# Performance work log

Hardware: AMD Instinct MI355X
Metric: run time of the kernel (lower is better)

## Reference

```python
import jax, jax.numpy as jnp
import numpy as np

EPS = 1e-5          # InstanceNorm2d default eps
SLOPE = 0.01        # LeakyReLU default negative_slope
C = 256


def setup_inputs() -> dict:
    key = jax.random.key(0)
    k = jax.random.split(key, 5)
    B, H, W = 8, 128, 128
    x = jax.random.normal(k[0], (B, C, H, W), dtype=jnp.float32)
    # attn: Conv2d(C, C//4, 1, bias=False) then Conv2d(C//4, C, 1, bias=False)
    attn_w1 = jax.random.normal(k[1], (C // 4, C), dtype=jnp.float32) * (1.0 / np.sqrt(C))
    attn_w2 = jax.random.normal(k[2], (C, C // 4), dtype=jnp.float32) * (1.0 / np.sqrt(C // 4))
    # refine: depthwise Conv2d(C, C, 3, padding=1, groups=C) with bias
    refine_w = jax.random.normal(k[3], (C, 1, 3, 3), dtype=jnp.float32) * (1.0 / 3.0)
    refine_b = jax.random.normal(k[4], (C,), dtype=jnp.float32) * 0.01
    return {"x": x, "attn_w1": attn_w1, "attn_w2": attn_w2,
            "refine_w": refine_w, "refine_b": refine_b}


def reference(x, attn_w1, attn_w2, refine_w, refine_b):
    # The torch module runs pywt wavedec2 -> waverec2 on x[b,c].detach().
    # With db2 (symmetric mode) and H,W divisible by 2^level, waverec2 is a
    # perfect-reconstruction identity and interpolate to (H,W) is a no-op,
    # so x_wave == stop_gradient(x) exactly.
    xw = jax.lax.stop_gradient(x)

    # --- channel attention (squeeze-excite with 1x1 convs == GEMMs) ---
    p = jnp.mean(xw, axis=(2, 3))                      # [B, C] global avg pool
    h = jax.nn.leaky_relu(p @ attn_w1.T, SLOPE)        # [B, C//4]
    a = jax.nn.sigmoid(h @ attn_w2.T)                  # [B, C]
    y = xw * a[:, :, None, None]

    # --- depthwise 3x3 refine conv ---
    y = jax.lax.conv_general_dilated(
        y, refine_w, window_strides=(1, 1), padding='SAME',
        feature_group_count=C,
        dimension_numbers=('NCHW', 'OIHW', 'NCHW'))
    y = y + refine_b[None, :, None, None]

    # --- InstanceNorm2d (affine=False, biased variance) ---
    mu = jnp.mean(y, axis=(2, 3), keepdims=True)
    var = jnp.mean(jnp.square(y - mu), axis=(2, 3), keepdims=True)
    y = (y - mu) * jax.lax.rsqrt(var + EPS)

    return jax.nn.leaky_relu(y, SLOPE)
```

## Files before the change

kernel.cpp:

```cpp
#include <hip/hip_runtime.h>
#include <hip/hip_bf16.h>
#include <math.h>

#define NPLANE 2048
#define HW     16384
#define WW     128
#define SLOPE  0.01f
#define EPS    1e-5f

typedef float v4f __attribute__((ext_vector_type(4)));

__device__ __forceinline__ void load_row(const float* __restrict__ xp, int r,
                                         int c4, int lane32,
                                         float4& m, float& L, float& R) {
    int rc = r;
    if (rc < 0) rc = 0;
    if (rc > 127) rc = 127;
    const float va = (r == rc) ? 1.f : 0.f;
    float4 v = *(const float4*)(xp + rc * WW + c4);
    m.x = v.x * va; m.y = v.y * va; m.z = v.z * va; m.w = v.w * va;
    L = __shfl_up(m.w, 1, 64);
    if (lane32 == 0) L = 0.f;
    R = __shfl_down(m.x, 1, 64);
    if (lane32 == 31) R = 0.f;
}

#define CONV4(o0, o1, o2, o3)                                                \
    float o0 = w_0*L0   + w_1*m0.x + w_2*m0.y                                \
             + w_3*L1   + w_4*m1.x + w_5*m1.y                                \
             + w_6*L2   + w_7*m2.x + w_8*m2.y;                               \
    float o1 = w_0*m0.x + w_1*m0.y + w_2*m0.z                                \
             + w_3*m1.x + w_4*m1.y + w_5*m1.z                                \
             + w_6*m2.x + w_7*m2.y + w_8*m2.z;                               \
    float o2 = w_0*m0.y + w_1*m0.z + w_2*m0.w                                \
             + w_3*m1.y + w_4*m1.z + w_5*m1.w                                \
             + w_6*m2.y + w_7*m2.z + w_8*m2.w;                               \
    float o3 = w_0*m0.z + w_1*m0.w + w_2*R0                                  \
             + w_3*m1.z + w_4*m1.w + w_5*R1                                  \
             + w_6*m2.z + w_7*m2.w + w_8*R2

#define SLIDE() do { m0 = m1; L0 = L1; R0 = R1; m1 = m2; L1 = L2; R1 = R2; } while (0)

__global__ __launch_bounds__(256, 8) void k_stats(const float* __restrict__ x,
                                                  const float* __restrict__ rw,
                                                  float* __restrict__ p,
                                                  float* __restrict__ cstats) {
    const int plane = blockIdx.x;
    const int ch = plane & 255;
    const float* xp = x + (size_t)plane * HW;
    const int lane32 = threadIdx.x & 31;
    const int c4 = lane32 * 4;
    const int r0 = (threadIdx.x >> 5) * 16;

    const float w_0 = rw[ch*9+0], w_1 = rw[ch*9+1], w_2 = rw[ch*9+2];
    const float w_3 = rw[ch*9+3], w_4 = rw[ch*9+4], w_5 = rw[ch*9+5];
    const float w_6 = rw[ch*9+6], w_7 = rw[ch*9+7], w_8 = rw[ch*9+8];

    float4 m0, m1, m2;
    float L0, R0, L1, R1, L2, R2;
    load_row(xp, r0 - 1, c4, lane32, m0, L0, R0);
    load_row(xp, r0,     c4, lane32, m1, L1, R1);

    float xs = 0.f, s = 0.f, sq = 0.f;
#pragma unroll 4
    for (int j = 0; j < 16; ++j) {
        load_row(xp, r0 + j + 1, c4, lane32, m2, L2, R2);
        CONV4(o0, o1, o2, o3);
        s  += (o0 + o1) + (o2 + o3);
        sq += o0*o0 + o1*o1 + o2*o2 + o3*o3;
        xs += (m1.x + m1.y) + (m1.z + m1.w);
        SLIDE();
    }

#pragma unroll
    for (int off = 32; off; off >>= 1) {
        xs += __shfl_down(xs, off, 64);
        s  += __shfl_down(s,  off, 64);
        sq += __shfl_down(sq, off, 64);
    }
    __shared__ float red[12];
    const int wave = threadIdx.x >> 6, lane = threadIdx.x & 63;
    if (lane == 0) { red[wave] = xs; red[4+wave] = s; red[8+wave] = sq; }
    __syncthreads();
    if (threadIdx.x == 0) {
        p[plane]            = ((red[0]+red[1]) + (red[2]+red[3])) * (1.f/(float)HW);
        cstats[plane*2]     = (red[4]+red[5]) + (red[6]+red[7]);
        cstats[plane*2 + 1] = (red[8]+red[9]) + (red[10]+red[11]);
    }
}

__global__ __launch_bounds__(256, 8) void k_out(const float* __restrict__ x,
                                                const float* __restrict__ w1,
                                                const float* __restrict__ w2,
                                                const float* __restrict__ rw,
                                                const float* __restrict__ p,
                                                const float* __restrict__ cstats,
                                                float* __restrict__ out) {
    __shared__ float hs[64];
    __shared__ float sh_mean, sh_scale;
    const int plane = blockIdx.x;
    const int b = plane >> 8, ch = plane & 255;

    {
        const int j = threadIdx.x >> 2, part = threadIdx.x & 3;
        const float4* pr = (const float4*)(p  + b * 256 + part * 64);
        const float4* wr = (const float4*)(w1 + j * 256 + part * 64);
        float acc = 0.f;
#pragma unroll
        for (int k = 0; k < 16; ++k) {
            float4 pv = pr[k], wv = wr[k];
            acc += pv.x*wv.x + pv.y*wv.y + pv.z*wv.z + pv.w*wv.w;
        }
        acc += __shfl_xor(acc, 1, 64);
        acc += __shfl_xor(acc, 2, 64);
        if (part == 0) hs[j] = acc > 0.f ? acc : SLOPE * acc;
    }
    __syncthreads();
    if (threadIdx.x < 64) {
        float v = w2[ch * 64 + threadIdx.x] * hs[threadIdx.x];
#pragma unroll
        for (int off = 32; off; off >>= 1) v += __shfl_down(v, off, 64);
        if (threadIdx.x == 0) {
            const float a  = 1.f / (1.f + expf(-v));
            const float mc = cstats[plane*2] * (1.f/(float)HW);
            const float vc = cstats[plane*2 + 1] * (1.f/(float)HW) - mc * mc;
            sh_mean  = mc;
            sh_scale = a * rsqrtf(a * a * vc + EPS);
        }
    }

    const float w_0 = rw[ch*9+0], w_1 = rw[ch*9+1], w_2 = rw[ch*9+2];
    const float w_3 = rw[ch*9+3], w_4 = rw[ch*9+4], w_5 = rw[ch*9+5];
    const float w_6 = rw[ch*9+6], w_7 = rw[ch*9+7], w_8 = rw[ch*9+8];

    __syncthreads();
    const float mean_c = sh_mean, scale = sh_scale;

    const float* xp = x + (size_t)plane * HW;
    float* op = out + (size_t)plane * HW;
    const int lane32 = threadIdx.x & 31;
    const int c4 = lane32 * 4;
    const int r0 = (threadIdx.x >> 5) * 16;

    float4 m0, m1, m2;
    float L0, R0, L1, R1, L2, R2;
    load_row(xp, r0 - 1, c4, lane32, m0, L0, R0);
    load_row(xp, r0,     c4, lane32, m1, L1, R1);

#pragma unroll 4
    for (int j = 0; j < 16; ++j) {
        load_row(xp, r0 + j + 1, c4, lane32, m2, L2, R2);
        CONV4(o0, o1, o2, o3);
        v4f res;
        float t0 = scale * (o0 - mean_c); res.x = t0 > 0.f ? t0 : SLOPE * t0;
        float t1 = scale * (o1 - mean_c); res.y = t1 > 0.f ? t1 : SLOPE * t1;
        float t2 = scale * (o2 - mean_c); res.z = t2 > 0.f ? t2 : SLOPE * t2;
        float t3 = scale * (o3 - mean_c); res.w = t3 > 0.f ? t3 : SLOPE * t3;
        __builtin_nontemporal_store(res, (v4f*)(op + (r0 + j) * WW + c4));
        SLIDE();
    }
}

extern "C" void kernel_launch(void* const* d_in, const int* in_sizes, int n_in,
                              void* d_out, int out_size, void* d_ws, size_t ws_size,
                              hipStream_t stream) {
    const float* x  = (const float*)d_in[0];
    const float* w1 = (const float*)d_in[1];
    const float* w2 = (const float*)d_in[2];
    const float* rw = (const float*)d_in[3];
    float* out = (float*)d_out;

    float* p      = (float*)d_ws;
    float* cstats = p + NPLANE;

    k_stats<<<NPLANE, 256, 0, stream>>>(x, rw, p, cstats);
    k_out  <<<NPLANE, 256, 0, stream>>>(x, w1, w2, rw, p, cstats, out);
}
```

Before: 276.0 us.

## Fuse stats and output kernels into one cooperative launch with grid sync

The two kernels become one cooperative kernel. It computes the conv statistics per plane, waits at a grid-wide barrier, then runs the squeeze-excite and the normalized conv output in the same launch. This removes the second launch and may let the second pass over x hit in cache because the same blocks reread their planes. It relies on all 2048 blocks being co-resident (8 per CU on 256 CUs); if the cooperative launch fails, it falls back to the original two launches.

```diff
diff --git a/kernel.cpp b/kernel.cpp
--- a/kernel.cpp
+++ b/kernel.cpp
@@ -1,6 +1,8 @@
 #include <hip/hip_runtime.h>
-#include <hip/hip_bf16.h>
+#include <hip/hip_cooperative_groups.h>
 #include <math.h>
+
+namespace cg = cooperative_groups;
 
 #define NPLANE 2048
 #define HW     16384
@@ -41,6 +43,115 @@
 
 #define SLIDE() do { m0 = m1; L0 = L1; R0 = R1; m1 = m2; L1 = L2; R1 = R2; } while (0)
 
+__global__ __launch_bounds__(256, 8) void k_fused(const float* __restrict__ x,
+                                                  const float* __restrict__ w1,
+                                                  const float* __restrict__ w2,
+                                                  const float* __restrict__ rw,
+                                                  float* __restrict__ p,
+                                                  float* __restrict__ cstats,
+                                                  float* __restrict__ out) {
+    __shared__ float red[12];
+    __shared__ float hs[64];
+    __shared__ float sh_mean, sh_scale;
+
+    const int plane = blockIdx.x;
+    const int b = plane >> 8, ch = plane & 255;
+    const float* xp = x + (size_t)plane * HW;
+    const int lane32 = threadIdx.x & 31;
+    const int c4 = lane32 * 4;
+    const int r0 = (threadIdx.x >> 5) * 16;
+
+    const float w_0 = rw[ch*9+0], w_1 = rw[ch*9+1], w_2 = rw[ch*9+2];
+    const float w_3 = rw[ch*9+3], w_4 = rw[ch*9+4], w_5 = rw[ch*9+5];
+    const float w_6 = rw[ch*9+6], w_7 = rw[ch*9+7], w_8 = rw[ch*9+8];
+
+    {
+        float4 m0, m1, m2;
+        float L0, R0, L1, R1, L2, R2;
+        load_row(xp, r0 - 1, c4, lane32, m0, L0, R0);
+        load_row(xp, r0,     c4, lane32, m1, L1, R1);
+
+        float xs = 0.f, s = 0.f, sq = 0.f;
+#pragma unroll 4
+        for (int j = 0; j < 16; ++j) {
+            load_row(xp, r0 + j + 1, c4, lane32, m2, L2, R2);
+            CONV4(o0, o1, o2, o3);
+            s  += (o0 + o1) + (o2 + o3);
+            sq += o0*o0 + o1*o1 + o2*o2 + o3*o3;
+            xs += (m1.x + m1.y) + (m1.z + m1.w);
+            SLIDE();
+        }
+
+#pragma unroll
+        for (int off = 32; off; off >>= 1) {
+            xs += __shfl_down(xs, off, 64);
+            s  += __shfl_down(s,  off, 64);
+            sq += __shfl_down(sq, off, 64);
+        }
+        const int wave = threadIdx.x >> 6, lane = threadIdx.x & 63;
+        if (lane == 0) { red[wave] = xs; red[4+wave] = s; red[8+wave] = sq; }
+        __syncthreads();
+        if (threadIdx.x == 0) {
+            p[plane]            = ((red[0]+red[1]) + (red[2]+red[3])) * (1.f/(float)HW);
+            cstats[plane*2]     = (red[4]+red[5]) + (red[6]+red[7]);
+            cstats[plane*2 + 1] = (red[8]+red[9]) + (red[10]+red[11]);
+        }
+    }
+
+    cg::this_grid().sync();
+
+    {
+        const int j = threadIdx.x >> 2, part = threadIdx.x & 3;
+        const float4* pr = (const float4*)(p  + b * 256 + part * 64);
+        const float4* wr = (const float4*)(w1 + j * 256 + part * 64);
+        float acc = 0.f;
+#pragma unroll
+        for (int k = 0; k < 16; ++k) {
+            float4 pv = pr[k], wv = wr[k];
+            acc += pv.x*wv.x + pv.y*wv.y + pv.z*wv.z + pv.w*wv.w;
+        }
+        acc += __shfl_xor(acc, 1, 64);
+        acc += __shfl_xor(acc, 2, 64);
+        if (part == 0) hs[j] = acc > 0.f ? acc : SLOPE * acc;
+    }
+    __syncthreads();
+    if (threadIdx.x < 64) {
+        float v = w2[ch * 64 + threadIdx.x] * hs[threadIdx.x];
+#pragma unroll
+        for (int off = 32; off; off >>= 1) v += __shfl_down(v, off, 64);
+        if (threadIdx.x == 0) {
+            const float a  = 1.f / (1.f + expf(-v));
+            const float mc = cstats[plane*2] * (1.f/(float)HW);
+            const float vc = cstats[plane*2 + 1] * (1.f/(float)HW) - mc * mc;
+            sh_mean  = mc;
+            sh_scale = a * rsqrtf(a * a * vc + EPS);
+        }
+    }
+    __syncthreads();
+    const float mean_c = sh_mean, scale = sh_scale;
+
+    float* op = out + (size_t)plane * HW;
+    {
+        float4 m0, m1, m2;
+        float L0, R0, L1, R1, L2, R2;
+        load_row(xp, r0 - 1, c4, lane32, m0, L0, R0);
+        load_row(xp, r0,     c4, lane32, m1, L1, R1);
+
+#pragma unroll 4
+        for (int j = 0; j < 16; ++j) {
+            load_row(xp, r0 + j + 1, c4, lane32, m2, L2, R2);
+            CONV4(o0, o1, o2, o3);
+            v4f res;
+            float t0 = scale * (o0 - mean_c); res.x = t0 > 0.f ? t0 : SLOPE * t0;
+            float t1 = scale * (o1 - mean_c); res.y = t1 > 0.f ? t1 : SLOPE * t1;
+            float t2 = scale * (o2 - mean_c); res.z = t2 > 0.f ? t2 : SLOPE * t2;
+            float t3 = scale * (o3 - mean_c); res.w = t3 > 0.f ? t3 : SLOPE * t3;
+            __builtin_nontemporal_store(res, (v4f*)(op + (r0 + j) * WW + c4));
+            SLIDE();
+        }
+    }
+}
+
 __global__ __launch_bounds__(256, 8) void k_stats(const float* __restrict__ x,
                                                   const float* __restrict__ rw,
                                                   float* __restrict__ p,
@@ -173,6 +284,13 @@
     float* p      = (float*)d_ws;
     float* cstats = p + NPLANE;
 
-    k_stats<<<NPLANE, 256, 0, stream>>>(x, rw, p, cstats);
-    k_out  <<<NPLANE, 256, 0, stream>>>(x, w1, w2, rw, p, cstats, out);
-}
+    void* args[] = {(void*)&x, (void*)&w1, (void*)&w2, (void*)&rw,
+                    (void*)&p, (void*)&cstats, (void*)&out};
+    hipError_t e = hipLaunchCooperativeKernel((const void*)k_fused,
+                                              dim3(NPLANE), dim3(256),
+                                              args, 0, stream);
+    if (e != hipSuccess) {
+        k_stats<<<NPLANE, 256, 0, stream>>>(x, rw, p, cstats);
+        k_out  <<<NPLANE, 256, 0, stream>>>(x, w1, w2, rw, p, cstats, out);
+    }
+}
```

Measured after the change: 448.6 us. 1.63x slower.

## Move conv statistics into output kernel, keeping conv results in registers

Applied to the files above, without the earlier changes.

The first kernel now only computes the per-plane mean of x with simple coalesced float4 loads and no convolution. The output kernel computes the depthwise conv once, keeps all 16 rows of results in registers, reduces sum and sum-of-squares across the block, then normalizes and stores. This removes the duplicated convolution in the stats pass. It raises register pressure (occupancy hint lowered to 4) and adds a block-wide barrier between compute and store.

```diff
diff --git a/kernel.cpp b/kernel.cpp
--- a/kernel.cpp
+++ b/kernel.cpp
@@ -1,5 +1,4 @@
 #include <hip/hip_runtime.h>
-#include <hip/hip_bf16.h>
 #include <math.h>
 
 #define NPLANE 2048
@@ -9,6 +8,8 @@
 #define EPS    1e-5f
 
 typedef float v4f __attribute__((ext_vector_type(4)));
+
+struct W9 { float w0,w1,w2,w3,w4,w5,w6,w7,w8; };
 
 __device__ __forceinline__ void load_row(const float* __restrict__ xp, int r,
                                          int c4, int lane32,
@@ -25,79 +26,34 @@
     if (lane32 == 31) R = 0.f;
 }
 
-#define CONV4(o0, o1, o2, o3)                                                \
-    float o0 = w_0*L0   + w_1*m0.x + w_2*m0.y                                \
-             + w_3*L1   + w_4*m1.x + w_5*m1.y                                \
-             + w_6*L2   + w_7*m2.x + w_8*m2.y;                               \
-    float o1 = w_0*m0.x + w_1*m0.y + w_2*m0.z                                \
-             + w_3*m1.x + w_4*m1.y + w_5*m1.z                                \
-             + w_6*m2.x + w_7*m2.y + w_8*m2.z;                               \
-    float o2 = w_0*m0.y + w_1*m0.z + w_2*m0.w                                \
-             + w_3*m1.y + w_4*m1.z + w_5*m1.w                                \
-             + w_6*m2.y + w_7*m2.z + w_8*m2.w;                               \
-    float o3 = w_0*m0.z + w_1*m0.w + w_2*R0                                  \
-             + w_3*m1.z + w_4*m1.w + w_5*R1                                  \
-             + w_6*m2.z + w_7*m2.w + w_8*R2
-
-#define SLIDE() do { m0 = m1; L0 = L1; R0 = R1; m1 = m2; L1 = L2; R1 = R2; } while (0)
-
-__global__ __launch_bounds__(256, 8) void k_stats(const float* __restrict__ x,
-                                                  const float* __restrict__ rw,
-                                                  float* __restrict__ p,
-                                                  float* __restrict__ cstats) {
+__global__ __launch_bounds__(256, 8) void k_mean(const float* __restrict__ x,
+                                                 float* __restrict__ p) {
     const int plane = blockIdx.x;
-    const int ch = plane & 255;
-    const float* xp = x + (size_t)plane * HW;
-    const int lane32 = threadIdx.x & 31;
-    const int c4 = lane32 * 4;
-    const int r0 = (threadIdx.x >> 5) * 16;
-
-    const float w_0 = rw[ch*9+0], w_1 = rw[ch*9+1], w_2 = rw[ch*9+2];
-    const float w_3 = rw[ch*9+3], w_4 = rw[ch*9+4], w_5 = rw[ch*9+5];
-    const float w_6 = rw[ch*9+6], w_7 = rw[ch*9+7], w_8 = rw[ch*9+8];
-
-    float4 m0, m1, m2;
-    float L0, R0, L1, R1, L2, R2;
-    load_row(xp, r0 - 1, c4, lane32, m0, L0, R0);
-    load_row(xp, r0,     c4, lane32, m1, L1, R1);
-
-    float xs = 0.f, s = 0.f, sq = 0.f;
-#pragma unroll 4
-    for (int j = 0; j < 16; ++j) {
-        load_row(xp, r0 + j + 1, c4, lane32, m2, L2, R2);
-        CONV4(o0, o1, o2, o3);
-        s  += (o0 + o1) + (o2 + o3);
-        sq += o0*o0 + o1*o1 + o2*o2 + o3*o3;
-        xs += (m1.x + m1.y) + (m1.z + m1.w);
-        SLIDE();
+    const float4* xp = (const float4*)(x + (size_t)plane * HW);
+    float xs = 0.f;
+#pragma unroll
+    for (int i = 0; i < 16; ++i) {
+        float4 v = xp[i * 256 + threadIdx.x];
+        xs += (v.x + v.y) + (v.z + v.w);
     }
-
 #pragma unroll
-    for (int off = 32; off; off >>= 1) {
-        xs += __shfl_down(xs, off, 64);
-        s  += __shfl_down(s,  off, 64);
-        sq += __shfl_down(sq, off, 64);
-    }
-    __shared__ float red[12];
-    const int wave = threadIdx.x >> 6, lane = threadIdx.x & 63;
-    if (lane == 0) { red[wave] = xs; red[4+wave] = s; red[8+wave] = sq; }
+    for (int off = 32; off; off >>= 1) xs += __shfl_down(xs, off, 64);
+    __shared__ float red[4];
+    if ((threadIdx.x & 63) == 0) red[threadIdx.x >> 6] = xs;
     __syncthreads();
-    if (threadIdx.x == 0) {
-        p[plane]            = ((red[0]+red[1]) + (red[2]+red[3])) * (1.f/(float)HW);
-        cstats[plane*2]     = (red[4]+red[5]) + (red[6]+red[7]);
-        cstats[plane*2 + 1] = (red[8]+red[9]) + (red[10]+red[11]);
-    }
+    if (threadIdx.x == 0)
+        p[plane] = ((red[0] + red[1]) + (red[2] + red[3])) * (1.f / (float)HW);
 }
 
-__global__ __launch_bounds__(256, 8) void k_out(const float* __restrict__ x,
+__global__ __launch_bounds__(256, 4) void k_out(const float* __restrict__ x,
                                                 const float* __restrict__ w1,
                                                 const float* __restrict__ w2,
                                                 const float* __restrict__ rw,
                                                 const float* __restrict__ p,
-                                                const float* __restrict__ cstats,
                                                 float* __restrict__ out) {
     __shared__ float hs[64];
-    __shared__ float sh_mean, sh_scale;
+    __shared__ float red[8];
+    __shared__ float sh_a, sh_mean, sh_scale;
     const int plane = blockIdx.x;
     const int b = plane >> 8, ch = plane & 255;
 
@@ -120,24 +76,14 @@
         float v = w2[ch * 64 + threadIdx.x] * hs[threadIdx.x];
 #pragma unroll
         for (int off = 32; off; off >>= 1) v += __shfl_down(v, off, 64);
-        if (threadIdx.x == 0) {
-            const float a  = 1.f / (1.f + expf(-v));
-            const float mc = cstats[plane*2] * (1.f/(float)HW);
-            const float vc = cstats[plane*2 + 1] * (1.f/(float)HW) - mc * mc;
-            sh_mean  = mc;
-            sh_scale = a * rsqrtf(a * a * vc + EPS);
-        }
+        if (threadIdx.x == 0) sh_a = 1.f / (1.f + expf(-v));
     }
 
-    const float w_0 = rw[ch*9+0], w_1 = rw[ch*9+1], w_2 = rw[ch*9+2];
-    const float w_3 = rw[ch*9+3], w_4 = rw[ch*9+4], w_5 = rw[ch*9+5];
-    const float w_6 = rw[ch*9+6], w_7 = rw[ch*9+7], w_8 = rw[ch*9+8];
-
-    __syncthreads();
-    const float mean_c = sh_mean, scale = sh_scale;
+    const W9 w = { rw[ch*9+0], rw[ch*9+1], rw[ch*9+2],
+                   rw[ch*9+3], rw[ch*9+4], rw[ch*9+5],
+                   rw[ch*9+6], rw[ch*9+7], rw[ch*9+8] };
 
     const float* xp = x + (size_t)plane * HW;
-    float* op = out + (size_t)plane * HW;
     const int lane32 = threadIdx.x & 31;
     const int c4 = lane32 * 4;
     const int r0 = (threadIdx.x >> 5) * 16;
@@ -147,17 +93,58 @@
     load_row(xp, r0 - 1, c4, lane32, m0, L0, R0);
     load_row(xp, r0,     c4, lane32, m1, L1, R1);
 
-#pragma unroll 4
+    v4f res[16];
+    float s = 0.f, sq = 0.f;
+#pragma unroll
     for (int j = 0; j < 16; ++j) {
         load_row(xp, r0 + j + 1, c4, lane32, m2, L2, R2);
-        CONV4(o0, o1, o2, o3);
-        v4f res;
-        float t0 = scale * (o0 - mean_c); res.x = t0 > 0.f ? t0 : SLOPE * t0;
-        float t1 = scale * (o1 - mean_c); res.y = t1 > 0.f ? t1 : SLOPE * t1;
-        float t2 = scale * (o2 - mean_c); res.z = t2 > 0.f ? t2 : SLOPE * t2;
-        float t3 = scale * (o3 - mean_c); res.w = t3 > 0.f ? t3 : SLOPE * t3;
-        __builtin_nontemporal_store(res, (v4f*)(op + (r0 + j) * WW + c4));
-        SLIDE();
+        float o0 = w.w0*L0   + w.w1*m0.x + w.w2*m0.y
+                 + w.w3*L1   + w.w4*m1.x + w.w5*m1.y
+                 + w.w6*L2   + w.w7*m2.x + w.w8*m2.y;
+        float o1 = w.w0*m0.x + w.w1*m0.y + w.w2*m0.z
+                 + w.w3*m1.x + w.w4*m1.y + w.w5*m1.z
+                 + w.w6*m2.x + w.w7*m2.y + w.w8*m2.z;
+        float o2 = w.w0*m0.y + w.w1*m0.z + w.w2*m0.w
+                 + w.w3*m1.y + w.w4*m1.z + w.w5*m1.w
+                 + w.w6*m2.y + w.w7*m2.z + w.w8*m2.w;
+        float o3 = w.w0*m0.z + w.w1*m0.w + w.w2*R0
+                 + w.w3*m1.z + w.w4*m1.w + w.w5*R1
+                 + w.w6*m2.z + w.w7*m2.w + w.w8*R2;
+        res[j].x = o0; res[j].y = o1; res[j].z = o2; res[j].w = o3;
+        s  += (o0 + o1) + (o2 + o3);
+        sq += o0*o0 + o1*o1 + o2*o2 + o3*o3;
+        m0 = m1; L0 = L1; R0 = R1; m1 = m2; L1 = L2; R1 = R2;
+    }
+
+#pragma unroll
+    for (int off = 32; off; off >>= 1) {
+        s  += __shfl_down(s,  off, 64);
+        sq += __shfl_down(sq, off, 64);
+    }
+    const int wave = threadIdx.x >> 6, lane = threadIdx.x & 63;
+    if (lane == 0) { red[wave] = s; red[4+wave] = sq; }
+    __syncthreads();
+    if (threadIdx.x == 0) {
+        const float S  = (red[0]+red[1]) + (red[2]+red[3]);
+        const float SQ = (red[4]+red[5]) + (red[6]+red[7]);
+        const float mc = S * (1.f/(float)HW);
+        const float vc = SQ * (1.f/(float)HW) - mc * mc;
+        const float a  = sh_a;
+        sh_mean  = mc;
+        sh_scale = a * rsqrtf(a * a * vc + EPS);
+    }
+    __syncthreads();
+    const float mean_c = sh_mean, scale = sh_scale;
+
+    float* op = out + (size_t)plane * HW;
+#pragma unroll
+    for (int j = 0; j < 16; ++j) {
+        v4f r = res[j], o;
+        float t0 = scale * (r.x - mean_c); o.x = t0 > 0.f ? t0 : SLOPE * t0;
+        float t1 = scale * (r.y - mean_c); o.y = t1 > 0.f ? t1 : SLOPE * t1;
+        float t2 = scale * (r.z - mean_c); o.z = t2 > 0.f ? t2 : SLOPE * t2;
+        float t3 = scale * (r.w - mean_c); o.w = t3 > 0.f ? t3 : SLOPE * t3;
+        __builtin_nontemporal_store(o, (v4f*)(op + (r0 + j) * WW + c4));
     }
 }
 
@@ -170,9 +157,8 @@
     const float* rw = (const float*)d_in[3];
     float* out = (float*)d_out;
 
-    float* p      = (float*)d_ws;
-    float* cstats = p + NPLANE;
+    float* p = (float*)d_ws;
 
-    k_stats<<<NPLANE, 256, 0, stream>>>(x, rw, p, cstats);
-    k_out  <<<NPLANE, 256, 0, stream>>>(x, w1, w2, rw, p, cstats, out);
+    k_mean<<<NPLANE, 256, 0, stream>>>(x, p);
+    k_out <<<NPLANE, 256, 0, stream>>>(x, w1, w2, rw, p, out);
 }
```

New measurement: 282.1 us. 2.2% more time.
